# Kernel optimization log

Measured on AMD Instinct MI355X. Metric: run time of the kernel, lower is better.

The kernel has to match this reference:

```python
import math
import jax, jax.numpy as jnp
import numpy as np

SHAPES = [(80, 80), (40, 40), (20, 20), (10, 10)]
BS, LQ, D, NH, NL, NP = 8, 1000, 256, 8, 4, 4
C = D // NH


def _offset_bias():
    # replicates _reset_parameters grid_init bias for sampling_offsets
    thetas = np.arange(NH, dtype=np.float32) * (2.0 * math.pi / NH)
    grid = np.stack([np.cos(thetas), np.sin(thetas)], -1)  # [NH,2]
    grid = grid / np.abs(grid).max(-1, keepdims=True)
    grid = np.tile(grid[:, None, None, :], (1, NL, NP, 1))  # [NH,NL,NP,2]
    for i in range(NP):
        grid[:, :, i, :] *= i + 1
    return jnp.asarray(grid.reshape(-1))


def setup_inputs() -> dict:
    key = jax.random.key(0)
    ks = jax.random.split(key, 8)
    len_v = sum(h * w for h, w in SHAPES)
    s = 1.0 / math.sqrt(D)
    starts = np.cumsum([0] + [h * w for h, w in SHAPES])[:-1]
    return {
        "query": jax.random.normal(ks[0], (BS, LQ, D), jnp.float32),
        "reference_points": jax.random.uniform(ks[1], (BS, LQ, NL, 2), jnp.float32),
        "value": jax.random.normal(ks[2], (BS, len_v, D), jnp.float32),
        "w_off": jax.random.normal(ks[3], (D, NH * NL * NP * 2), jnp.float32) * 0.01,
        "b_off": _offset_bias(),
        "w_attn": jax.random.normal(ks[4], (D, NH * NL * NP), jnp.float32) * 0.01,
        "b_attn": jnp.zeros((NH * NL * NP,), jnp.float32),
        "w_v": jax.random.normal(ks[5], (D, D), jnp.float32) * s,
        "b_v": jnp.zeros((D,), jnp.float32),
        "w_o": jax.random.normal(ks[6], (D, D), jnp.float32) * s,
        "b_o": jnp.zeros((D,), jnp.float32),
        "value_spatial_shapes": jnp.array(SHAPES, jnp.int32),
        "value_level_start_index": jnp.array(starts, jnp.int32),
    }


def _sample(img, grid, H, W):
    # bilinear grid_sample, padding_mode='zeros', align_corners=False
    # img: [B, C, H*W], grid: [B, Q, P, 2] in [-1, 1] -> out [B, C, Q, P]
    x = (grid[..., 0] + 1.0) * (W * 0.5) - 0.5
    y = (grid[..., 1] + 1.0) * (H * 0.5) - 0.5
    x0 = jnp.floor(x)
    y0 = jnp.floor(y)
    fx = x - x0
    fy = y - y0
    x0i = x0.astype(jnp.int32)
    y0i = y0.astype(jnp.int32)

    def gather(xi, yi, w):
        valid = (xi >= 0) & (xi < W) & (yi >= 0) & (yi < H)
        idx = jnp.clip(yi, 0, H - 1) * W + jnp.clip(xi, 0, W - 1)
        B, Q, P = idx.shape
        g = jax.vmap(lambda im, ix: im[:, ix])(img, idx.reshape(B, Q * P))  # [B,C,QP]
        return g.reshape(B, -1, Q, P) * (w * valid)[:, None]

    return (gather(x0i, y0i, (1 - fx) * (1 - fy))
            + gather(x0i + 1, y0i, fx * (1 - fy))
            + gather(x0i, y0i + 1, (1 - fx) * fy)
            + gather(x0i + 1, y0i + 1, fx * fy))


def _forward(query, reference_points, value, w_off, b_off, w_attn, b_attn,
             w_v, b_v, w_o, b_o, shapes):
    bs, lq, _ = query.shape
    v = (value @ w_v + b_v).reshape(bs, -1, NH, C)  # [bs, len_v, NH, C]
    off = (query @ w_off + b_off).reshape(bs, lq, NH, NL, NP, 2)
    attn = jax.nn.softmax((query @ w_attn + b_attn).reshape(bs, lq, NH, NL * NP), axis=-1)
    attn = attn.reshape(bs, lq, NH, NL, NP)
    # offset normalizer is spatial_shapes flipped -> (W, H) per level
    norm = jnp.array([[w, h] for h, w in shapes], dtype=query.dtype)  # [NL,2]
    loc = reference_points[:, :, None, :, None, :] + off / norm[None, None, None, :, None, :]
    grids = 2.0 * loc - 1.0  # [bs,lq,NH,NL,NP,2]
    start = 0
    sampled = []
    for lvl, (H, W) in enumerate(shapes):
        v_l = v[:, start:start + H * W].transpose(0, 2, 3, 1).reshape(bs * NH, C, H * W)
        g_l = grids[:, :, :, lvl].transpose(0, 2, 1, 3, 4).reshape(bs * NH, lq, NP, 2)
        sampled.append(_sample(v_l, g_l, H, W))  # [bs*NH, C, lq, NP]
        start += H * W
    samp = jnp.stack(sampled, axis=3).reshape(bs * NH, C, lq, NL * NP)
    aw = attn.transpose(0, 2, 1, 3, 4).reshape(bs * NH, 1, lq, NL * NP)
    out = (samp * aw).sum(-1).reshape(bs, NH * C, lq).transpose(0, 2, 1)  # [bs,lq,D]
    return out @ w_o + b_o


def reference(query, reference_points, value, w_off, b_off, w_attn, b_attn,
              w_v, b_v, w_o, b_o, value_spatial_shapes, value_level_start_index):
    shapes = [tuple(int(x) for x in r) for r in np.asarray(value_spatial_shapes)]
    return _forward(query, reference_points, value, w_off, b_off, w_attn, b_attn,
                    w_v, b_v, w_o, b_o, shapes)
```

## Files before the change

### kernel.cpp

```cpp
#include <hip/hip_runtime.h>
#include <hip/hip_bf16.h>
#include <math.h>

#define BS     8
#define LQ     1000
#define DMODEL 256
#define NH     8
#define NLV    4
#define NPT    4
#define LEN_V  8500
#define NQ     (BS*LQ)
#define MV     (BS*LEN_V)
#define KS     8

typedef __attribute__((ext_vector_type(8))) short short8;
typedef __attribute__((ext_vector_type(4))) float floatx4;

static __device__ __forceinline__ unsigned short f2bf(float f) {
    __hip_bfloat16 h = __float2bfloat16(f);
    return __builtin_bit_cast(unsigned short, h);
}
static __device__ __forceinline__ float asf(unsigned int u) {
    return __builtin_bit_cast(float, u);
}

static __device__ __forceinline__ void dma16(const unsigned short* g, unsigned short* lds) {
    __builtin_amdgcn_global_load_lds(
        (const __attribute__((address_space(1))) unsigned int*)g,
        (__attribute__((address_space(3))) unsigned int*)lds,
        16, 0, 0);
}

template <bool A32>
static __device__ __forceinline__ void gemm_tile(
    const void* __restrict__ Aptr, const unsigned short* __restrict__ Bfrag,
    const float* __restrict__ bias1, const float* __restrict__ bias2, int nsplit,
    void* __restrict__ Cptr, int M, int N, int bn, int bm,
    bool outbf, unsigned short* As )
{
    const int tid = threadIdx.x;
    const int l   = tid & 63;
    const int w   = tid >> 6;
    const int lm  = l & 15;
    const int lk  = l >> 4;
    const int x7  = lm & 7;

    auto aoff = [&](int j) -> size_t {
        const int slot = j * 256 + tid;
        const int row  = slot >> 5;
        const int gc   = (slot & 31) ^ (row & 7);
        int grow = bm * 64 + row; grow = grow < M ? grow : M - 1;
        return (size_t)grow * 256 + gc * 8;
    };

    float4 ra[8][2];
    if constexpr (A32) {
        #pragma unroll
        for (int j = 0; j < 8; ++j) {
            const float* s = (const float*)Aptr + aoff(j);
            ra[j][0] = *(const float4*)s;
            ra[j][1] = *(const float4*)(s + 4);
        }
    } else {
        #pragma unroll
        for (int j = 0; j < 8; ++j)
            dma16((const unsigned short*)Aptr + aoff(j),
                  &As[(j * 256 + w * 64) * 8]);
    }

    short8 Bf[2][KS];
    const int u0 = bn * 8 + w * 2;
    #pragma unroll
    for (int j = 0; j < 2; ++j)
        #pragma unroll
        for (int s = 0; s < KS; ++s)
            Bf[j][s] = *(const short8*)(Bfrag + ((size_t)((u0 + j) * KS + s) * 64 + l) * 8);

    if constexpr (A32) {
        #pragma unroll
        for (int j = 0; j < 8; ++j) {
            short8 o;
            o[0] = (short)f2bf(ra[j][0].x); o[1] = (short)f2bf(ra[j][0].y);
            o[2] = (short)f2bf(ra[j][0].z); o[3] = (short)f2bf(ra[j][0].w);
            o[4] = (short)f2bf(ra[j][1].x); o[5] = (short)f2bf(ra[j][1].y);
            o[6] = (short)f2bf(ra[j][1].z); o[7] = (short)f2bf(ra[j][1].w);
            *(short8*)&As[(j * 256 + tid) * 8] = o;
        }
    } else {
        __builtin_amdgcn_s_waitcnt(0);
    }
    __syncthreads();

    floatx4 acc[4][2];
    #pragma unroll
    for (int i = 0; i < 4; ++i)
        #pragma unroll
        for (int j = 0; j < 2; ++j)
            #pragma unroll
            for (int r = 0; r < 4; ++r) acc[i][j][r] = 0.f;

    #pragma unroll
    for (int s = 0; s < KS; ++s) {
        short8 afr[4];
        #pragma unroll
        for (int i = 0; i < 4; ++i)
            afr[i] = *(const short8*)(
                &As[(i * 16 + lm) * 256 + (((s * 4 + lk) ^ x7)) * 8]);
        #pragma unroll
        for (int i = 0; i < 4; ++i)
            #pragma unroll
            for (int j = 0; j < 2; ++j)
                acc[i][j] = __builtin_amdgcn_mfma_f32_16x16x32_bf16(
                                afr[i], Bf[j][s], acc[i][j], 0, 0, 0);
    }

    #pragma unroll
    for (int j = 0; j < 2; ++j) {
        const int col = bn * 128 + w * 32 + j * 16 + lm;
        const float bv = (bias2 != nullptr && col >= nsplit) ? bias2[col - nsplit]
                                                             : bias1[col];
        #pragma unroll
        for (int i = 0; i < 4; ++i) {
            const int rbase = bm * 64 + i * 16 + lk * 4;
            #pragma unroll
            for (int r = 0; r < 4; ++r) {
                const int row = rbase + r;
                if (row < M) {
                    const float v = acc[i][j][r] + bv;
                    if (outbf)
                        ((unsigned short*)Cptr)[(size_t)row * N + col] = f2bf(v);
                    else
                        ((float*)Cptr)[(size_t)row * N + col] = v;
                }
            }
        }
    }
}

__global__ __launch_bounds__(256, 4) void gemm_fused(
    const float* __restrict__ value, const float* __restrict__ query,
    const unsigned short* __restrict__ wv_f, const unsigned short* __restrict__ woa_f,
    const float* __restrict__ b_v, const float* __restrict__ b_off,
    const float* __restrict__ b_attn,
    unsigned short* __restrict__ v_proj, float* __restrict__ offattn)
{
    __shared__ unsigned short As[16384];
    int bx = blockIdx.x;
    if (bx < 2126) {
        gemm_tile<true>(value, wv_f, b_v, nullptr, 1 << 30,
                        v_proj, MV, 256, bx & 1, bx >> 1, true, As);
    } else {
        bx -= 2126;
        gemm_tile<true>(query, woa_f, b_off, b_attn, 256,
                        offattn, NQ, 384, bx % 3, bx / 3, false, As);
    }
}

__global__ __launch_bounds__(256, 4) void gemm_out(
    const unsigned short* __restrict__ out_pre, const unsigned short* __restrict__ wo_f,
    const float* __restrict__ b_o, float* __restrict__ out)
{
    __shared__ unsigned short As[16384];
    gemm_tile<false>(out_pre, wo_f, b_o, nullptr, 1 << 30,
                     out, NQ, 256, blockIdx.x & 1, blockIdx.x >> 1, false, As);
}

__global__ __launch_bounds__(256) void prep_w(
    const float* __restrict__ w_v, const float* __restrict__ w_off,
    const float* __restrict__ w_attn, const float* __restrict__ w_o,
    unsigned short* __restrict__ wv_f, unsigned short* __restrict__ woa_f,
    unsigned short* __restrict__ wo_f)
{
    const int gid = blockIdx.x * 256 + threadIdx.x;
    int chunk, mode;
    if (gid < 8192)               { chunk = gid;         mode = 0; }
    else if (gid < 8192 + 12288)  { chunk = gid - 8192;  mode = 1; }
    else                          { chunk = gid - 20480; mode = 2; }
    const int l = chunk & 63, s = (chunk >> 6) & 7, u = chunk >> 9;
    short8 o;
    #pragma unroll
    for (int j = 0; j < 8; ++j) {
        const int k = s * 32 + (l >> 4) * 8 + j;
        const int n = u * 16 + (l & 15);
        float v;
        if (mode == 0)      v = w_v[k * 256 + n];
        else if (mode == 1) v = (n < 256) ? w_off[k * 256 + n] : w_attn[k * 128 + (n - 256)];
        else                v = w_o[k * 256 + n];
        o[j] = (short)f2bf(v);
    }
    unsigned short* dp = (mode == 0 ? wv_f : mode == 1 ? woa_f : wo_f)
                         + ((size_t)(u * 8 + s) * 64 + l) * 8;
    *(short8*)dp = o;
}

__global__ __launch_bounds__(512) void ms_sample_split(
    const unsigned short* __restrict__ v,
    const float* __restrict__ offattn,
    const float* __restrict__ refp,
    unsigned short* __restrict__ out_pre)
{
    __shared__ float offx_s[8][16][8];
    __shared__ float offy_s[8][16][8];
    __shared__ float atw_s [8][16][8];
    __shared__ float ref_s [8][8];
    __shared__ float part  [8][32][9];

    const int tid  = threadIdx.x;
    const int bswz = blockIdx.x & 7;
    const int iq0  = bswz * 1000 + (blockIdx.x >> 3) * 8;

    if (tid < 64) {
        const int q = tid >> 3, h = tid & 7;
        const float* rowp = offattn + (size_t)(iq0 + q) * 384;
        float lg[16];
        float m = -1e30f;
        #pragma unroll
        for (int i = 0; i < 16; ++i) { lg[i] = rowp[256 + h * 16 + i]; m = fmaxf(m, lg[i]); }
        float s = 0.f;
        #pragma unroll
        for (int i = 0; i < 16; ++i) { lg[i] = __expf(lg[i] - m); s += lg[i]; }
        const float inv = 1.f / s;
        #pragma unroll
        for (int i = 0; i < 16; ++i) atw_s[q][i][h] = lg[i] * inv;
        #pragma unroll
        for (int i = 0; i < 16; ++i) {
            offx_s[q][i][h] = rowp[(h * 16 + i) * 2 + 0];
            offy_s[q][i][h] = rowp[(h * 16 + i) * 2 + 1];
        }
        if (h == 0) {
            #pragma unroll
            for (int i = 0; i < 8; ++i) ref_s[q][i] = refp[(size_t)(iq0 + q) * 8 + i];
        }
    }
    __syncthreads();

    const int q8   = tid >> 6;
    const int half = (tid >> 5) & 1;
    const int sub  = tid & 31;
    const int h    = sub >> 2;
    const int oct  = sub & 3;

    float acc[8] = {0.f, 0.f, 0.f, 0.f, 0.f, 0.f, 0.f, 0.f};
    const unsigned short* vb = v + (size_t)bswz * LEN_V * 256 + h * 32 + oct * 8;
    const int Hs[4] = {80, 40, 20, 10};
    const int st[4] = {0, 6400, 8000, 8400};

    #pragma unroll
    for (int li = 0; li < 2; ++li) {
        const int lvl = half * 2 + li;
        const int W = Hs[lvl];
        const float bx = ref_s[q8][lvl * 2 + 0] * (float)W - 0.5f;
        const float by = ref_s[q8][lvl * 2 + 1] * (float)W - 0.5f;
        const unsigned short* vl = vb + (size_t)st[lvl] * 256;
        #pragma unroll
        for (int p = 0; p < NPT; ++p) {
            const int lp = lvl * 4 + p;
            const float x  = bx + offx_s[q8][lp][h];
            const float y  = by + offy_s[q8][lp][h];
            const float at = atw_s[q8][lp][h];
            const float x0f = floorf(x), y0f = floorf(y);
            const float fx = x - x0f, fy = y - y0f;
            const int x0 = (int)x0f, y0 = (int)y0f;
            const int x1 = x0 + 1,   y1 = y0 + 1;
            const int cx0 = min(max(x0, 0), W - 1);
            const int cx1 = min(max(x1, 0), W - 1);
            const int cy0 = min(max(y0, 0), W - 1);
            const int cy1 = min(max(y1, 0), W - 1);
            const float vx0 = (x0 >= 0 && x0 < W) ? 1.f : 0.f;
            const float vx1 = (x1 >= 0 && x1 < W) ? 1.f : 0.f;
            const float vy0 = (y0 >= 0 && y0 < W) ? 1.f : 0.f;
            const float vy1 = (y1 >= 0 && y1 < W) ? 1.f : 0.f;
            const float w00 = at * (1.f - fx) * (1.f - fy) * vx0 * vy0;
            const float w01 = at * fx * (1.f - fy) * vx1 * vy0;
            const float w10 = at * (1.f - fx) * fy * vx0 * vy1;
            const float w11 = at * fx * fy * vx1 * vy1;
            const unsigned short* r0 = vl + (size_t)(cy0 * W) * 256;
            const unsigned short* r1 = vl + (size_t)(cy1 * W) * 256;
            const uint4 d00 = *(const uint4*)(r0 + (size_t)cx0 * 256);
            const uint4 d01 = *(const uint4*)(r0 + (size_t)cx1 * 256);
            const uint4 d10 = *(const uint4*)(r1 + (size_t)cx0 * 256);
            const uint4 d11 = *(const uint4*)(r1 + (size_t)cx1 * 256);
            acc[0] += w00 * asf(d00.x << 16) + w01 * asf(d01.x << 16)
                    + w10 * asf(d10.x << 16) + w11 * asf(d11.x << 16);
            acc[1] += w00 * asf(d00.x & 0xffff0000u) + w01 * asf(d01.x & 0xffff0000u)
                    + w10 * asf(d10.x & 0xffff0000u) + w11 * asf(d11.x & 0xffff0000u);
            acc[2] += w00 * asf(d00.y << 16) + w01 * asf(d01.y << 16)
                    + w10 * asf(d10.y << 16) + w11 * asf(d11.y << 16);
            acc[3] += w00 * asf(d00.y & 0xffff0000u) + w01 * asf(d01.y & 0xffff0000u)
                    + w10 * asf(d10.y & 0xffff0000u) + w11 * asf(d11.y & 0xffff0000u);
            acc[4] += w00 * asf(d00.z << 16) + w01 * asf(d01.z << 16)
                    + w10 * asf(d10.z << 16) + w11 * asf(d11.z << 16);
            acc[5] += w00 * asf(d00.z & 0xffff0000u) + w01 * asf(d01.z & 0xffff0000u)
                    + w10 * asf(d10.z & 0xffff0000u) + w11 * asf(d11.z & 0xffff0000u);
            acc[6] += w00 * asf(d00.w << 16) + w01 * asf(d01.w << 16)
                    + w10 * asf(d10.w << 16) + w11 * asf(d11.w << 16);
            acc[7] += w00 * asf(d00.w & 0xffff0000u) + w01 * asf(d01.w & 0xffff0000u)
                    + w10 * asf(d10.w & 0xffff0000u) + w11 * asf(d11.w & 0xffff0000u);
        }
    }

    if (half == 1) {
        #pragma unroll
        for (int j = 0; j < 8; ++j) part[q8][sub][j] = acc[j];
    }
    __syncthreads();
    if (half == 0) {
        short8 o;
        #pragma unroll
        for (int j = 0; j < 8; ++j) o[j] = (short)f2bf(acc[j] + part[q8][sub][j]);
        *(short8*)(out_pre + (size_t)(iq0 + q8) * 256 + sub * 8) = o;
    }
}

extern "C" void kernel_launch(void* const* d_in, const int* in_sizes, int n_in,
                              void* d_out, int out_size, void* d_ws, size_t ws_size,
                              hipStream_t stream)
{
    const float* query  = (const float*)d_in[0];
    const float* refp   = (const float*)d_in[1];
    const float* value  = (const float*)d_in[2];
    const float* w_off  = (const float*)d_in[3];
    const float* b_off  = (const float*)d_in[4];
    const float* w_attn = (const float*)d_in[5];
    const float* b_attn = (const float*)d_in[6];
    const float* w_v    = (const float*)d_in[7];
    const float* b_v    = (const float*)d_in[8];
    const float* w_o    = (const float*)d_in[9];
    const float* b_o    = (const float*)d_in[10];
    (void)d_in[11]; (void)d_in[12];

    float* out = (float*)d_out;

    char* ws = (char*)d_ws;
    unsigned short* v_proj  = (unsigned short*)ws;
    float*          offattn = (float*)(ws + 34816000);
    unsigned short* out_pre = (unsigned short*)(ws + 47104000);
    unsigned short* wv_f    = (unsigned short*)(ws + 51200000);
    unsigned short* woa_f   = (unsigned short*)(ws + 51331072);
    unsigned short* wo_f    = (unsigned short*)(ws + 51527680);

    dim3 blk(256);

    hipLaunchKernelGGL(prep_w, dim3(112), blk, 0, stream,
                       w_v, w_off, w_attn, w_o, wv_f, woa_f, wo_f);
    hipLaunchKernelGGL(gemm_fused, dim3(2501), blk, 0, stream,
                       value, query, wv_f, woa_f, b_v, b_off, b_attn, v_proj, offattn);
    hipLaunchKernelGGL(ms_sample_split, dim3(1000), dim3(512), 0, stream,
                       v_proj, offattn, refp, out_pre);
    hipLaunchKernelGGL(gemm_out, dim3(250), blk, 0, stream,
                       out_pre, wo_f, b_o, out);
}
```

Measured before the change: 190.6 us.

## Halve GEMM tile rows, DMA fp32 A into LDS, split sampler by head halves

GEMM tiles shrink from 64 to 32 rows, which doubles the block count for all three GEMM launches. The fp32 A operand is now copied straight into LDS with global_load_lds under an XOR swizzle, and the bf16 conversion moves to fragment load time, replacing the register staging and convert-then-store path. The sampling kernel is split into 256-thread blocks that each handle four heads, doubling the grid. The aim is more parallelism and latency hiding on a load-bound pipeline. In exchange, fp32 LDS traffic and conversion work per MFMA step go up, and the M-bound row checks are removed because the 32-row tiles divide both M sizes exactly.

```diff
diff --git a/kernel.cpp b/kernel.cpp
--- a/kernel.cpp
+++ b/kernel.cpp
@@ -24,7 +24,7 @@
     return __builtin_bit_cast(float, u);
 }
 
-static __device__ __forceinline__ void dma16(const unsigned short* g, unsigned short* lds) {
+static __device__ __forceinline__ void dma16(const void* g, void* lds) {
     __builtin_amdgcn_global_load_lds(
         (const __attribute__((address_space(1))) unsigned int*)g,
         (__attribute__((address_space(3))) unsigned int*)lds,
@@ -32,11 +32,11 @@
 }
 
 template <bool A32>
-static __device__ __forceinline__ void gemm_tile(
+static __device__ __forceinline__ void gemm_tile32(
     const void* __restrict__ Aptr, const unsigned short* __restrict__ Bfrag,
     const float* __restrict__ bias1, const float* __restrict__ bias2, int nsplit,
-    void* __restrict__ Cptr, int M, int N, int bn, int bm,
-    bool outbf, unsigned short* As )
+    void* __restrict__ Cptr, int N, int bn, int bm,
+    bool outbf, unsigned short* As)
 {
     const int tid = threadIdx.x;
     const int l   = tid & 63;
@@ -45,27 +45,27 @@
     const int lk  = l >> 4;
     const int x7  = lm & 7;
 
-    auto aoff = [&](int j) -> size_t {
-        const int slot = j * 256 + tid;
-        const int row  = slot >> 5;
-        const int gc   = (slot & 31) ^ (row & 7);
-        int grow = bm * 64 + row; grow = grow < M ? grow : M - 1;
-        return (size_t)grow * 256 + gc * 8;
-    };
-
-    float4 ra[8][2];
     if constexpr (A32) {
+        const float* A = (const float*)Aptr;
+        float* As_f = (float*)As;
         #pragma unroll
         for (int j = 0; j < 8; ++j) {
-            const float* s = (const float*)Aptr + aoff(j);
-            ra[j][0] = *(const float4*)s;
-            ra[j][1] = *(const float4*)(s + 4);
+            const int slot = j * 256 + tid;
+            const int row  = slot >> 6;
+            const int gsrc = (slot & 63) ^ (row & 15);
+            dma16(A + (size_t)(bm * 32 + row) * 256 + gsrc * 4,
+                  As_f + (size_t)(j * 256 + w * 64) * 4);
         }
     } else {
-        #pragma unroll
-        for (int j = 0; j < 8; ++j)
-            dma16((const unsigned short*)Aptr + aoff(j),
+        const unsigned short* A = (const unsigned short*)Aptr;
+        #pragma unroll
+        for (int j = 0; j < 4; ++j) {
+            const int slot = j * 256 + tid;
+            const int row  = slot >> 5;
+            const int gc   = (slot & 31) ^ (row & 7);
+            dma16(A + (size_t)(bm * 32 + row) * 256 + gc * 8,
                   &As[(j * 256 + w * 64) * 8]);
+        }
     }
 
     short8 Bf[2][KS];
@@ -76,24 +76,12 @@
         for (int s = 0; s < KS; ++s)
             Bf[j][s] = *(const short8*)(Bfrag + ((size_t)((u0 + j) * KS + s) * 64 + l) * 8);
 
-    if constexpr (A32) {
-        #pragma unroll
-        for (int j = 0; j < 8; ++j) {
-            short8 o;
-            o[0] = (short)f2bf(ra[j][0].x); o[1] = (short)f2bf(ra[j][0].y);
-            o[2] = (short)f2bf(ra[j][0].z); o[3] = (short)f2bf(ra[j][0].w);
-            o[4] = (short)f2bf(ra[j][1].x); o[5] = (short)f2bf(ra[j][1].y);
-            o[6] = (short)f2bf(ra[j][1].z); o[7] = (short)f2bf(ra[j][1].w);
-            *(short8*)&As[(j * 256 + tid) * 8] = o;
-        }
-    } else {
-        __builtin_amdgcn_s_waitcnt(0);
-    }
+    __builtin_amdgcn_s_waitcnt(0);
     __syncthreads();
 
-    floatx4 acc[4][2];
-    #pragma unroll
-    for (int i = 0; i < 4; ++i)
+    floatx4 acc[2][2];
+    #pragma unroll
+    for (int i = 0; i < 2; ++i)
         #pragma unroll
         for (int j = 0; j < 2; ++j)
             #pragma unroll
@@ -101,13 +89,26 @@
 
     #pragma unroll
     for (int s = 0; s < KS; ++s) {
-        short8 afr[4];
-        #pragma unroll
-        for (int i = 0; i < 4; ++i)
-            afr[i] = *(const short8*)(
-                &As[(i * 16 + lm) * 256 + (((s * 4 + lk) ^ x7)) * 8]);
-        #pragma unroll
-        for (int i = 0; i < 4; ++i)
+        short8 afr[2];
+        #pragma unroll
+        for (int i = 0; i < 2; ++i) {
+            if constexpr (A32) {
+                const float* As_f = (const float*)As;
+                const int row = i * 16 + lm;
+                const int cb  = s * 8 + lk * 2;
+                const float4 a0 = *(const float4*)&As_f[row * 256 + ((cb    ) ^ lm) * 4];
+                const float4 a1 = *(const float4*)&As_f[row * 256 + ((cb + 1) ^ lm) * 4];
+                afr[i][0] = (short)f2bf(a0.x); afr[i][1] = (short)f2bf(a0.y);
+                afr[i][2] = (short)f2bf(a0.z); afr[i][3] = (short)f2bf(a0.w);
+                afr[i][4] = (short)f2bf(a1.x); afr[i][5] = (short)f2bf(a1.y);
+                afr[i][6] = (short)f2bf(a1.z); afr[i][7] = (short)f2bf(a1.w);
+            } else {
+                afr[i] = *(const short8*)(
+                    &As[(i * 16 + lm) * 256 + (((s * 4 + lk) ^ x7)) * 8]);
+            }
+        }
+        #pragma unroll
+        for (int i = 0; i < 2; ++i)
             #pragma unroll
             for (int j = 0; j < 2; ++j)
                 acc[i][j] = __builtin_amdgcn_mfma_f32_16x16x32_bf16(
@@ -120,18 +121,15 @@
         const float bv = (bias2 != nullptr && col >= nsplit) ? bias2[col - nsplit]
                                                              : bias1[col];
         #pragma unroll
-        for (int i = 0; i < 4; ++i) {
-            const int rbase = bm * 64 + i * 16 + lk * 4;
+        for (int i = 0; i < 2; ++i) {
+            const int rbase = bm * 32 + i * 16 + lk * 4;
             #pragma unroll
             for (int r = 0; r < 4; ++r) {
-                const int row = rbase + r;
-                if (row < M) {
-                    const float v = acc[i][j][r] + bv;
-                    if (outbf)
-                        ((unsigned short*)Cptr)[(size_t)row * N + col] = f2bf(v);
-                    else
-                        ((float*)Cptr)[(size_t)row * N + col] = v;
-                }
+                const float v = acc[i][j][r] + bv;
+                if (outbf)
+                    ((unsigned short*)Cptr)[(size_t)(rbase + r) * N + col] = f2bf(v);
+                else
+                    ((float*)Cptr)[(size_t)(rbase + r) * N + col] = v;
             }
         }
     }
@@ -146,13 +144,13 @@
 {
     __shared__ unsigned short As[16384];
     int bx = blockIdx.x;
-    if (bx < 2126) {
-        gemm_tile<true>(value, wv_f, b_v, nullptr, 1 << 30,
-                        v_proj, MV, 256, bx & 1, bx >> 1, true, As);
+    if (bx < 4250) {
+        gemm_tile32<true>(value, wv_f, b_v, nullptr, 1 << 30,
+                          v_proj, 256, bx & 1, bx >> 1, true, As);
     } else {
-        bx -= 2126;
-        gemm_tile<true>(query, woa_f, b_off, b_attn, 256,
-                        offattn, NQ, 384, bx % 3, bx / 3, false, As);
+        bx -= 4250;
+        gemm_tile32<true>(query, woa_f, b_off, b_attn, 256,
+                          offattn, 384, bx % 3, bx / 3, false, As);
     }
 }
 
@@ -160,9 +158,9 @@
     const unsigned short* __restrict__ out_pre, const unsigned short* __restrict__ wo_f,
     const float* __restrict__ b_o, float* __restrict__ out)
 {
-    __shared__ unsigned short As[16384];
-    gemm_tile<false>(out_pre, wo_f, b_o, nullptr, 1 << 30,
-                     out, NQ, 256, blockIdx.x & 1, blockIdx.x >> 1, false, As);
+    __shared__ unsigned short As[8192];
+    gemm_tile32<false>(out_pre, wo_f, b_o, nullptr, 1 << 30,
+                       out, 256, blockIdx.x & 1, blockIdx.x >> 1, false, As);
 }
 
 __global__ __launch_bounds__(256) void prep_w(
@@ -193,24 +191,27 @@
     *(short8*)dp = o;
 }
 
-__global__ __launch_bounds__(512) void ms_sample_split(
+__global__ __launch_bounds__(256) void ms_sample_half(
     const unsigned short* __restrict__ v,
     const float* __restrict__ offattn,
     const float* __restrict__ refp,
     unsigned short* __restrict__ out_pre)
 {
-    __shared__ float offx_s[8][16][8];
-    __shared__ float offy_s[8][16][8];
-    __shared__ float atw_s [8][16][8];
+    __shared__ float offx_s[8][16][4];
+    __shared__ float offy_s[8][16][4];
+    __shared__ float atw_s [8][16][4];
     __shared__ float ref_s [8][8];
-    __shared__ float part  [8][32][9];
+    __shared__ float part  [8][16][9];
 
     const int tid  = threadIdx.x;
-    const int bswz = blockIdx.x & 7;
-    const int iq0  = bswz * 1000 + (blockIdx.x >> 3) * 8;
-
-    if (tid < 64) {
-        const int q = tid >> 3, h = tid & 7;
+    const int bid  = blockIdx.x;
+    const int hh   = (bid >= 1000) ? 1 : 0;
+    const int bb   = hh ? bid - 1000 : bid;
+    const int bswz = bb & 7;
+    const int iq0  = bswz * 1000 + (bb >> 3) * 8;
+
+    if (tid < 32) {
+        const int q = tid >> 2, h4 = tid & 3, h = hh * 4 + h4;
         const float* rowp = offattn + (size_t)(iq0 + q) * 384;
         float lg[16];
         float m = -1e30f;
@@ -221,33 +222,33 @@
         for (int i = 0; i < 16; ++i) { lg[i] = __expf(lg[i] - m); s += lg[i]; }
         const float inv = 1.f / s;
         #pragma unroll
-        for (int i = 0; i < 16; ++i) atw_s[q][i][h] = lg[i] * inv;
+        for (int i = 0; i < 16; ++i) atw_s[q][i][h4] = lg[i] * inv;
         #pragma unroll
         for (int i = 0; i < 16; ++i) {
-            offx_s[q][i][h] = rowp[(h * 16 + i) * 2 + 0];
-            offy_s[q][i][h] = rowp[(h * 16 + i) * 2 + 1];
-        }
-        if (h == 0) {
-            #pragma unroll
-            for (int i = 0; i < 8; ++i) ref_s[q][i] = refp[(size_t)(iq0 + q) * 8 + i];
-        }
+            offx_s[q][i][h4] = rowp[(h * 16 + i) * 2 + 0];
+            offy_s[q][i][h4] = rowp[(h * 16 + i) * 2 + 1];
+        }
+    }
+    if (tid < 8) {
+        #pragma unroll
+        for (int i = 0; i < 8; ++i) ref_s[tid][i] = refp[(size_t)(iq0 + tid) * 8 + i];
     }
     __syncthreads();
 
-    const int q8   = tid >> 6;
-    const int half = (tid >> 5) & 1;
-    const int sub  = tid & 31;
-    const int h    = sub >> 2;
-    const int oct  = sub & 3;
+    const int q8  = tid >> 5;
+    const int lh  = (tid >> 4) & 1;
+    const int sub = tid & 15;
+    const int h4  = sub >> 2;
+    const int oct = sub & 3;
 
     float acc[8] = {0.f, 0.f, 0.f, 0.f, 0.f, 0.f, 0.f, 0.f};
-    const unsigned short* vb = v + (size_t)bswz * LEN_V * 256 + h * 32 + oct * 8;
+    const unsigned short* vb = v + (size_t)bswz * LEN_V * 256 + (hh * 4 + h4) * 32 + oct * 8;
     const int Hs[4] = {80, 40, 20, 10};
     const int st[4] = {0, 6400, 8000, 8400};
 
     #pragma unroll
     for (int li = 0; li < 2; ++li) {
-        const int lvl = half * 2 + li;
+        const int lvl = lh * 2 + li;
         const int W = Hs[lvl];
         const float bx = ref_s[q8][lvl * 2 + 0] * (float)W - 0.5f;
         const float by = ref_s[q8][lvl * 2 + 1] * (float)W - 0.5f;
@@ -255,9 +256,9 @@
         #pragma unroll
         for (int p = 0; p < NPT; ++p) {
             const int lp = lvl * 4 + p;
-            const float x  = bx + offx_s[q8][lp][h];
-            const float y  = by + offy_s[q8][lp][h];
-            const float at = atw_s[q8][lp][h];
+            const float x  = bx + offx_s[q8][lp][h4];
+            const float y  = by + offy_s[q8][lp][h4];
+            const float at = atw_s[q8][lp][h4];
             const float x0f = floorf(x), y0f = floorf(y);
             const float fx = x - x0f, fy = y - y0f;
             const int x0 = (int)x0f, y0 = (int)y0f;
@@ -299,16 +300,16 @@
         }
     }
 
-    if (half == 1) {
+    if (lh == 1) {
         #pragma unroll
         for (int j = 0; j < 8; ++j) part[q8][sub][j] = acc[j];
     }
     __syncthreads();
-    if (half == 0) {
+    if (lh == 0) {
         short8 o;
         #pragma unroll
         for (int j = 0; j < 8; ++j) o[j] = (short)f2bf(acc[j] + part[q8][sub][j]);
-        *(short8*)(out_pre + (size_t)(iq0 + q8) * 256 + sub * 8) = o;
+        *(short8*)(out_pre + (size_t)(iq0 + q8) * 256 + (hh * 4 + h4) * 32 + oct * 8) = o;
     }
 }
 
@@ -343,10 +344,10 @@
 
     hipLaunchKernelGGL(prep_w, dim3(112), blk, 0, stream,
                        w_v, w_off, w_attn, w_o, wv_f, woa_f, wo_f);
-    hipLaunchKernelGGL(gemm_fused, dim3(2501), blk, 0, stream,
+    hipLaunchKernelGGL(gemm_fused, dim3(5000), blk, 0, stream,
                        value, query, wv_f, woa_f, b_v, b_off, b_attn, v_proj, offattn);
-    hipLaunchKernelGGL(ms_sample_split, dim3(1000), dim3(512), 0, stream,
+    hipLaunchKernelGGL(ms_sample_half, dim3(2000), blk, 0, stream,
                        v_proj, offattn, refp, out_pre);
-    hipLaunchKernelGGL(gemm_out, dim3(250), blk, 0, stream,
+    hipLaunchKernelGGL(gemm_out, dim3(500), blk, 0, stream,
                        out_pre, wo_f, b_o, out);
 }
```

Result: slower. 195.1 us (+2.4%).

## Fuse output projection GEMM into sampling kernel via per-block MFMA

Applied to the files above, without the earlier changes.

The output projection is moved into the sampling kernel. Each 8-query block writes its bf16 sampled rows into LDS, pads them to 16 rows with zeros, and runs a 16x16x32 bf16 MFMA against w_o fragments read from global memory. This drops the separate gemm_out launch and the out_pre round trip through global memory. In exchange, half of each MFMA tile is wasted on padding and each block re-reads the full w_o (mostly from cache). Launch bounds also change (gemm_fused occupancy hint from 4 to 3, sampler hint set to 4).

```diff
diff --git a/kernel.cpp b/kernel.cpp
--- a/kernel.cpp
+++ b/kernel.cpp
@@ -24,16 +24,8 @@
     return __builtin_bit_cast(float, u);
 }
 
-static __device__ __forceinline__ void dma16(const unsigned short* g, unsigned short* lds) {
-    __builtin_amdgcn_global_load_lds(
-        (const __attribute__((address_space(1))) unsigned int*)g,
-        (__attribute__((address_space(3))) unsigned int*)lds,
-        16, 0, 0);
-}
-
-template <bool A32>
 static __device__ __forceinline__ void gemm_tile(
-    const void* __restrict__ Aptr, const unsigned short* __restrict__ Bfrag,
+    const float* __restrict__ Aptr, const unsigned short* __restrict__ Bfrag,
     const float* __restrict__ bias1, const float* __restrict__ bias2, int nsplit,
     void* __restrict__ Cptr, int M, int N, int bn, int bm,
     bool outbf, unsigned short* As )
@@ -54,18 +46,11 @@
     };
 
     float4 ra[8][2];
-    if constexpr (A32) {
-        #pragma unroll
-        for (int j = 0; j < 8; ++j) {
-            const float* s = (const float*)Aptr + aoff(j);
-            ra[j][0] = *(const float4*)s;
-            ra[j][1] = *(const float4*)(s + 4);
-        }
-    } else {
-        #pragma unroll
-        for (int j = 0; j < 8; ++j)
-            dma16((const unsigned short*)Aptr + aoff(j),
-                  &As[(j * 256 + w * 64) * 8]);
+    #pragma unroll
+    for (int j = 0; j < 8; ++j) {
+        const float* s = Aptr + aoff(j);
+        ra[j][0] = *(const float4*)s;
+        ra[j][1] = *(const float4*)(s + 4);
     }
 
     short8 Bf[2][KS];
@@ -76,18 +61,14 @@
         for (int s = 0; s < KS; ++s)
             Bf[j][s] = *(const short8*)(Bfrag + ((size_t)((u0 + j) * KS + s) * 64 + l) * 8);
 
-    if constexpr (A32) {
-        #pragma unroll
-        for (int j = 0; j < 8; ++j) {
-            short8 o;
-            o[0] = (short)f2bf(ra[j][0].x); o[1] = (short)f2bf(ra[j][0].y);
-            o[2] = (short)f2bf(ra[j][0].z); o[3] = (short)f2bf(ra[j][0].w);
-            o[4] = (short)f2bf(ra[j][1].x); o[5] = (short)f2bf(ra[j][1].y);
-            o[6] = (short)f2bf(ra[j][1].z); o[7] = (short)f2bf(ra[j][1].w);
-            *(short8*)&As[(j * 256 + tid) * 8] = o;
-        }
-    } else {
-        __builtin_amdgcn_s_waitcnt(0);
+    #pragma unroll
+    for (int j = 0; j < 8; ++j) {
+        short8 o;
+        o[0] = (short)f2bf(ra[j][0].x); o[1] = (short)f2bf(ra[j][0].y);
+        o[2] = (short)f2bf(ra[j][0].z); o[3] = (short)f2bf(ra[j][0].w);
+        o[4] = (short)f2bf(ra[j][1].x); o[5] = (short)f2bf(ra[j][1].y);
+        o[6] = (short)f2bf(ra[j][1].z); o[7] = (short)f2bf(ra[j][1].w);
+        *(short8*)&As[(j * 256 + tid) * 8] = o;
     }
     __syncthreads();
 
@@ -137,7 +118,7 @@
     }
 }
 
-__global__ __launch_bounds__(256, 4) void gemm_fused(
+__global__ __launch_bounds__(256, 3) void gemm_fused(
     const float* __restrict__ value, const float* __restrict__ query,
     const unsigned short* __restrict__ wv_f, const unsigned short* __restrict__ woa_f,
     const float* __restrict__ b_v, const float* __restrict__ b_off,
@@ -147,22 +128,13 @@
     __shared__ unsigned short As[16384];
     int bx = blockIdx.x;
     if (bx < 2126) {
-        gemm_tile<true>(value, wv_f, b_v, nullptr, 1 << 30,
-                        v_proj, MV, 256, bx & 1, bx >> 1, true, As);
+        gemm_tile(value, wv_f, b_v, nullptr, 1 << 30,
+                  v_proj, MV, 256, bx & 1, bx >> 1, true, As);
     } else {
         bx -= 2126;
-        gemm_tile<true>(query, woa_f, b_off, b_attn, 256,
-                        offattn, NQ, 384, bx % 3, bx / 3, false, As);
-    }
-}
-
-__global__ __launch_bounds__(256, 4) void gemm_out(
-    const unsigned short* __restrict__ out_pre, const unsigned short* __restrict__ wo_f,
-    const float* __restrict__ b_o, float* __restrict__ out)
-{
-    __shared__ unsigned short As[16384];
-    gemm_tile<false>(out_pre, wo_f, b_o, nullptr, 1 << 30,
-                     out, NQ, 256, blockIdx.x & 1, blockIdx.x >> 1, false, As);
+        gemm_tile(query, woa_f, b_off, b_attn, 256,
+                  offattn, NQ, 384, bx % 3, bx / 3, false, As);
+    }
 }
 
 __global__ __launch_bounds__(256) void prep_w(
@@ -193,21 +165,31 @@
     *(short8*)dp = o;
 }
 
-__global__ __launch_bounds__(512) void ms_sample_split(
+__global__ __launch_bounds__(512, 4) void ms_sample_out(
     const unsigned short* __restrict__ v,
     const float* __restrict__ offattn,
     const float* __restrict__ refp,
-    unsigned short* __restrict__ out_pre)
+    const unsigned short* __restrict__ wo_f,
+    const float* __restrict__ b_o,
+    float* __restrict__ out)
 {
     __shared__ float offx_s[8][16][8];
     __shared__ float offy_s[8][16][8];
     __shared__ float atw_s [8][16][8];
     __shared__ float ref_s [8][8];
     __shared__ float part  [8][32][9];
+    __shared__ unsigned short pA[16][256];
 
     const int tid  = threadIdx.x;
     const int bswz = blockIdx.x & 7;
     const int iq0  = bswz * 1000 + (blockIdx.x >> 3) * 8;
+
+    {
+        const int row = 8 + (tid >> 6);
+        const int c4  = (tid & 63) * 4;
+        ushort4 z; z.x = 0; z.y = 0; z.z = 0; z.w = 0;
+        *(ushort4*)&pA[row][c4] = z;
+    }
 
     if (tid < 64) {
         const int q = tid >> 3, h = tid & 7;
@@ -308,7 +290,43 @@
         short8 o;
         #pragma unroll
         for (int j = 0; j < 8; ++j) o[j] = (short)f2bf(acc[j] + part[q8][sub][j]);
-        *(short8*)(out_pre + (size_t)(iq0 + q8) * 256 + sub * 8) = o;
+        *(short8*)&pA[q8][sub * 8] = o;
+    }
+    __syncthreads();
+
+    const int l  = tid & 63;
+    const int w8 = tid >> 6;
+    const int lm = l & 15;
+    const int lk = l >> 4;
+
+    floatx4 oacc[2];
+    #pragma unroll
+    for (int j = 0; j < 2; ++j)
+        #pragma unroll
+        for (int r = 0; r < 4; ++r) oacc[j][r] = 0.f;
+
+    #pragma unroll
+    for (int s = 0; s < KS; ++s) {
+        const short8 a = *(const short8*)&pA[lm][(s * 4 + lk) * 8];
+        #pragma unroll
+        for (int j = 0; j < 2; ++j) {
+            const short8 b = *(const short8*)(
+                wo_f + ((size_t)((w8 * 2 + j) * KS + s) * 64 + l) * 8);
+            oacc[j] = __builtin_amdgcn_mfma_f32_16x16x32_bf16(a, b, oacc[j], 0, 0, 0);
+        }
+    }
+
+    if (lk < 2) {
+        #pragma unroll
+        for (int j = 0; j < 2; ++j) {
+            const int col = w8 * 32 + j * 16 + lm;
+            const float bo = b_o[col];
+            #pragma unroll
+            for (int r = 0; r < 4; ++r) {
+                const int q = lk * 4 + r;
+                out[(size_t)(iq0 + q) * 256 + col] = oacc[j][r] + bo;
+            }
+        }
     }
 }
 
@@ -334,10 +352,9 @@
     char* ws = (char*)d_ws;
     unsigned short* v_proj  = (unsigned short*)ws;
     float*          offattn = (float*)(ws + 34816000);
-    unsigned short* out_pre = (unsigned short*)(ws + 47104000);
-    unsigned short* wv_f    = (unsigned short*)(ws + 51200000);
-    unsigned short* woa_f   = (unsigned short*)(ws + 51331072);
-    unsigned short* wo_f    = (unsigned short*)(ws + 51527680);
+    unsigned short* wv_f    = (unsigned short*)(ws + 47104000);
+    unsigned short* woa_f   = (unsigned short*)(ws + 47235072);
+    unsigned short* wo_f    = (unsigned short*)(ws + 47431680);
 
     dim3 blk(256);
 
@@ -345,8 +362,6 @@
                        w_v, w_off, w_attn, w_o, wv_f, woa_f, wo_f);
     hipLaunchKernelGGL(gemm_fused, dim3(2501), blk, 0, stream,
                        value, query, wv_f, woa_f, b_v, b_off, b_attn, v_proj, offattn);
-    hipLaunchKernelGGL(ms_sample_split, dim3(1000), dim3(512), 0, stream,
-                       v_proj, offattn, refp, out_pre);
-    hipLaunchKernelGGL(gemm_out, dim3(250), blk, 0, stream,
-                       out_pre, wo_f, b_o, out);
-}
+    hipLaunchKernelGGL(ms_sample_out, dim3(1000), dim3(512), 0, stream,
+                       v_proj, offattn, refp, wo_f, b_o, out);
+}
```

New measurement: 301.0 us. 1.58x slower.
